# Kernel tuning notes

Hardware: AMD Instinct MI355X
Metric: run time of the kernel (lower is better)

The kernel has to match this reference:

```python
import jax, jax.numpy as jnp
import numpy as np

B, P, N = 2, 8192, 24
C1, C2 = 32, 32
K, A = 13, 12  # kernel points (12 anchors + center), rotation anchors


def _icosahedron_vs():
    phi = (1.0 + np.sqrt(5.0)) / 2.0
    v = []
    for s1 in (1.0, -1.0):
        for s2 in (1.0, -1.0):
            v.append([0.0, s1, s2 * phi])
            v.append([s1, s2 * phi, 0.0])
            v.append([s2 * phi, 0.0, s1])
    v = np.array(v, dtype=np.float32)
    return v / np.linalg.norm(v, axis=1, keepdims=True)


def setup_inputs() -> dict:
    key = jax.random.key(0)
    ks = jax.random.split(key, 6)
    rng = np.random.RandomState(0)
    vertices = jax.random.normal(ks[0], (B, P, 3), jnp.float32)
    neighbor_index = jax.random.randint(ks[1], (B, P, N), 0, P)
    feature_map = jax.random.normal(ks[2], (B, C1, K, P, A), jnp.float32)
    W = jax.random.normal(ks[3], (C2, C1, 36), jnp.float32) * 0.05
    bias = jax.random.normal(ks[4], (C2, 5), jnp.float32) * 0.05
    k_pos_w = jax.random.normal(ks[5], (C2, 36), jnp.float32) * 0.1
    vs = jnp.asarray(_icosahedron_vs())
    # precomputed rotation-group trace index buffers (valid-range stand-ins for
    # the fr.get_relativeV_index / idx_map precomputation in the original repo)
    idx_map = jnp.asarray(rng.randint(0, 36, size=(K * A,)), jnp.int32)          # [156] -> 36 classes
    trace_idxv_rot = jnp.asarray(np.stack([rng.permutation(K) for _ in range(A)]), jnp.int32)  # [A(r), K]
    trace_idx_rot = jnp.asarray(np.stack([rng.permutation(A) for _ in range(A)]), jnp.int32)   # [A(r), A]
    lvl = jnp.asarray(np.concatenate([rng.randint(0, 4, size=(A,)), np.array([4])]), jnp.int32)  # [K] shell level per kernel point
    return dict(neighbor_index=neighbor_index, vertices=vertices, feature_map=feature_map,
                W=W, bias=bias, k_pos_w=k_pos_w, vs=vs, idx_map=idx_map,
                trace_idxv_rot=trace_idxv_rot, trace_idx_rot=trace_idx_rot, lvl=lvl)


def reference(neighbor_index, vertices, feature_map, W, bias, k_pos_w, vs,
              idx_map, trace_idxv_rot, trace_idx_rot, lvl):
    c2, c1, _ = W.shape
    # unit-normalized neighbor directions: [b, p, n, 3]
    nbr = jax.vmap(lambda v, i: v[i])(vertices, neighbor_index)
    d = nbr - vertices[:, :, None, :]
    ndn = d / jnp.maximum(jnp.linalg.norm(d, axis=-1, keepdims=True), 1e-12)
    # expand the 36 equivariance classes to the full (k, a) kernel grid
    k_pos_w_ori = k_pos_w[:, idx_map].reshape(c2, K, A)        # [d, k, a]
    W_re = W[:, :, idx_map].reshape(c2, c1, K, A)              # [d, c, k, a]
    # rotate kernel-point and anchor axes per output rotation r (gather by trace idx)
    Ik = trace_idxv_rot[:, :, None]   # [r, k, 1], values in [0, K)
    Ia = trace_idx_rot[:, None, :]    # [r, 1, a], values in [0, A)
    W_eff = jnp.transpose(W_re[:, :, Ik, Ia], (0, 1, 3, 4, 2))   # [d, c, k, a, r]
    k_eff = jnp.transpose(k_pos_w_ori[:, Ik, Ia], (0, 2, 3, 1))  # [d, k, a, r]
    # learned kernel-point positions on S2 and positional weights vs local geometry
    k_pos_ori = jnp.einsum('dka,ac->dkc', k_pos_w_ori, vs)
    k_pos_ori = k_pos_ori / jnp.maximum(jnp.linalg.norm(k_pos_ori, axis=-1, keepdims=True), 1e-12)
    mean_dir = ndn.mean(axis=2)                                  # [b, p, 3]
    pw = jax.nn.relu(jnp.einsum('bpc,dkc->bdpk', mean_dir, k_pos_ori))
    # equivariant conv: small per-point matmul over (c, a) per kernel point, then k-weighted sum
    WT = W_eff * k_eff[:, None]                                  # [d, c, k, a, r]
    agg = jnp.einsum('dckar,bckpa->bdkpr', WT, feature_map)
    out = jnp.einsum('bdkpr,bdpk->bdpr', agg, pw)
    bias_eff = bias[:, lvl][:, trace_idxv_rot].sum(axis=-1)      # [d, r]
    return jax.nn.relu(out + bias_eff[None, :, None, :])
```

## Files before the change

kernel.cpp:

```cpp
#include <hip/hip_runtime.h>
#include <cstdint>
#include <cstddef>

#define B_   2
#define P_   8192
#define NN_  24
#define C1_  32
#define C2_  32
#define K_   13
#define A_   12
#define DR_  384
#define CA_  384
#define PT_  32
#define BPAD 408

typedef __attribute__((ext_vector_type(8))) short short8;
typedef __attribute__((ext_vector_type(4))) float floatx4;

__device__ __forceinline__ unsigned short f2bf(float f) {
    union { float f; unsigned int u; } v; v.f = f;
    unsigned int u = v.u;
    return (unsigned short)((u + 0x7fffu + ((u >> 16) & 1u)) >> 16);
}


__global__ void build_wt(const float* __restrict__ W, const float* __restrict__ kpw,
                         const int* __restrict__ idx_map, const int* __restrict__ tivr,
                         const int* __restrict__ tir, unsigned short* __restrict__ WT2) {
    int id = blockIdx.x * 256 + threadIdx.x;
    const int TOT = K_ * DR_ * CA_;
    if (id >= TOT) return;
    int ca = id % CA_;
    int t1 = id / CA_;
    int dr = t1 % DR_;
    int k  = t1 / DR_;
    int d = dr / 12, r = dr % 12;
    int c = ca / 12, a = ca % 12;
    int kk = tivr[r * K_ + k];
    int ia = tir[r * A_ + a];
    int m  = idx_map[kk * A_ + ia];
    WT2[id] = f2bf(W[(d * C1_ + c) * 36 + m] * kpw[d * 36 + m]);
}

__global__ void build_md(const int* __restrict__ nbr, const float* __restrict__ verts,
                         float* __restrict__ md) {
    int t = blockIdx.x * 256 + threadIdx.x;
    if (t >= B_ * P_) return;
    const float* vp = verts + (size_t)t * 3;
    float vx = vp[0], vy = vp[1], vz = vp[2];
    int b = t / P_;
    const int* np = nbr + (size_t)t * NN_;
    float ax = 0.f, ay = 0.f, az = 0.f;
    for (int n = 0; n < NN_; n++) {
        int j = np[n];
        const float* vq = verts + ((size_t)b * P_ + j) * 3;
        float dx = vq[0] - vx, dy = vq[1] - vy, dz = vq[2] - vz;
        float nn = sqrtf(dx * dx + dy * dy + dz * dz);
        float inv = 1.f / fmaxf(nn, 1e-12f);
        ax += dx * inv; ay += dy * inv; az += dz * inv;
    }
    const float s = 1.f / 24.f;
    md[t * 3 + 0] = ax * s; md[t * 3 + 1] = ay * s; md[t * 3 + 2] = az * s;
}

__global__ void build_kpo(const float* __restrict__ kpw, const int* __restrict__ idx_map,
                          const float* __restrict__ vs, float* __restrict__ kpo) {
    int t = blockIdx.x * 64 + threadIdx.x;
    if (t >= C2_ * K_) return;
    int d = t / K_, k = t % K_;
    float x = 0.f, y = 0.f, z = 0.f;
    for (int a = 0; a < A_; a++) {
        float w = kpw[d * 36 + idx_map[k * A_ + a]];
        x += w * vs[a * 3 + 0]; y += w * vs[a * 3 + 1]; z += w * vs[a * 3 + 2];
    }
    float nn = sqrtf(x * x + y * y + z * z);
    float inv = 1.f / fmaxf(nn, 1e-12f);
    kpo[t * 3 + 0] = x * inv; kpo[t * 3 + 1] = y * inv; kpo[t * 3 + 2] = z * inv;
}

__global__ void build_be(const float* __restrict__ bias, const int* __restrict__ lvl,
                         const int* __restrict__ tivr, float* __restrict__ be) {
    int t = blockIdx.x * 64 + threadIdx.x;
    if (t >= DR_) return;
    int d = t / 12, r = t % 12;
    float s = 0.f;
    for (int k = 0; k < K_; k++) s += bias[d * 5 + lvl[tivr[r * K_ + k]]];
    be[t] = s;
}

__global__ __launch_bounds__(256, 2) void main_gemm(
    const float* __restrict__ fm, const unsigned short* __restrict__ WT,
    const float* __restrict__ md, const float* __restrict__ kpo,
    const float* __restrict__ be, float* __restrict__ out) {

    __shared__ __attribute__((aligned(16))) unsigned short Bs[2][PT_][BPAD];
    __shared__ float pwS[2][PT_][C2_];
    __shared__ float mdS[PT_][3];
    __shared__ float kpoS[C2_ * K_ * 3];
    __shared__ float biasS[DR_];

    const int tid  = threadIdx.x;
    const int bid  = blockIdx.x;
    const int b    = bid >> 8;
    const int p0   = (bid & 255) << 5;
    const int lane = tid & 63;
    const int wid  = tid >> 6;
    const int rowm = lane & 15;
    const int quad = lane >> 4;

    float4 pf[12];
    int pf_c[12], pf_jj[12];
    #pragma unroll
    for (int j = 0; j < 12; j++) {
        int f = j * 256 + tid;
        pf_c[j]  = f / 96;
        pf_jj[j] = f - pf_c[j] * 96;
    }

    #define LOAD_PF(kk)                                                                  \
        { _Pragma("unroll")                                                              \
          for (int j = 0; j < 12; j++) {                                                 \
            const float4* src = (const float4*)(fm +                                     \
                ((((size_t)b * C1_ + pf_c[j]) * K_ + (kk)) * P_ + p0) * A_) + pf_jj[j];  \
            pf[j] = *src;                                                                \
          } }

    #define STORE_PF(bufw)                                                               \
        { _Pragma("unroll")                                                              \
          for (int j = 0; j < 12; j++) {                                                 \
            int pl = pf_jj[j] / 3, aseg = (pf_jj[j] - pl * 3) * 4;                       \
            ushort4 pk = make_ushort4(f2bf(pf[j].x), f2bf(pf[j].y),                      \
                                      f2bf(pf[j].z), f2bf(pf[j].w));                     \
            *(ushort4*)&Bs[bufw][pl][pf_c[j] * A_ + aseg] = pk;                          \
          } }

    #define CALC_PW(bufw, kk)                                                            \
        { for (int i = tid; i < C2_ * PT_; i += 256) {                                   \
            int d = i >> 5, pl = i & 31;                                                 \
            const float* kv = &kpoS[(d * K_ + (kk)) * 3];                                \
            float s = mdS[pl][0] * kv[0] + mdS[pl][1] * kv[1] + mdS[pl][2] * kv[2];      \
            pwS[bufw][pl][d] = fmaxf(s, 0.f);                                            \
          } }

    const unsigned short* awbase = WT + (size_t)(wid * 96 + rowm) * CA_ + quad * 8;
    #define LOAD_A(dst, kk, ch)                                                          \
        { const unsigned short* ap = awbase + (size_t)(kk) * (DR_ * CA_) + (ch) * 32;    \
          _Pragma("unroll")                                                              \
          for (int mt = 0; mt < 6; mt++) dst[mt] = *(const short8*)(ap + mt * 16 * CA_); }

    for (int i = tid; i < PT_ * 3; i += 256) {
        int p = i / 3, c = i % 3;
        mdS[p][c] = md[((size_t)b * P_ + p0 + p) * 3 + c];
    }
    for (int i = tid; i < C2_ * K_ * 3; i += 256) kpoS[i] = kpo[i];
    for (int i = tid; i < DR_; i += 256) biasS[i] = be[i];

    floatx4 acc_o[6][2];
    floatx4 acc_k[6][2];
    #pragma unroll
    for (int mt = 0; mt < 6; mt++)
        #pragma unroll
        for (int nt = 0; nt < 2; nt++) { acc_o[mt][nt] = (floatx4)0.f; acc_k[mt][nt] = (floatx4)0.f; }

    short8 abuf[2][6];

    LOAD_PF(0);
    __syncthreads();
    STORE_PF(0);
    CALC_PW(0, 0);
    LOAD_A(abuf[0], 0, 0);
    LOAD_PF(1);

    for (int k = 0; k < K_; k++) {
        const int buf = k & 1;
        __syncthreads();

        #pragma unroll
        for (int ch = 0; ch < 12; ch++) {
            if (ch < 11) LOAD_A(abuf[(ch + 1) & 1], k, ch + 1);
            short8 bfr[2];
            #pragma unroll
            for (int nt = 0; nt < 2; nt++)
                bfr[nt] = *(const short8*)(&Bs[buf][nt * 16 + rowm][ch * 32 + quad * 8]);
            const short8* af = abuf[ch & 1];
            #pragma unroll
            for (int mt = 0; mt < 6; mt++)
                #pragma unroll
                for (int nt = 0; nt < 2; nt++)
                    acc_k[mt][nt] = __builtin_amdgcn_mfma_f32_16x16x32_bf16(af[mt], bfr[nt], acc_k[mt][nt], 0, 0, 0);
        }

        #pragma unroll
        for (int mt = 0; mt < 6; mt++) {
            int drb = wid * 96 + mt * 16 + quad * 4;
            #pragma unroll
            for (int reg = 0; reg < 4; reg++) {
                int d = (drb + reg) / 12;
                #pragma unroll
                for (int nt = 0; nt < 2; nt++) {
                    float pv = pwS[buf][nt * 16 + rowm][d];
                    acc_o[mt][nt][reg] += pv * acc_k[mt][nt][reg];
                    acc_k[mt][nt][reg] = 0.f;
                }
            }
        }

        if (k + 1 < K_) {
            STORE_PF(buf ^ 1);
            CALC_PW(buf ^ 1, k + 1);
            LOAD_A(abuf[0], k + 1, 0);
        }
        if (k + 2 < K_) LOAD_PF(k + 2);
    }

    #pragma unroll
    for (int mt = 0; mt < 6; mt++) {
        #pragma unroll
        for (int reg = 0; reg < 4; reg++) {
            int dr = wid * 96 + mt * 16 + quad * 4 + reg;
            int d = dr / 12, r = dr - d * 12;
            #pragma unroll
            for (int nt = 0; nt < 2; nt++) {
                int p = p0 + nt * 16 + rowm;
                float v = acc_o[mt][nt][reg] + biasS[dr];
                out[(((size_t)b * C2_ + d) * P_ + p) * A_ + r] = fmaxf(v, 0.f);
            }
        }
    }
}

extern "C" void kernel_launch(void* const* d_in, const int* in_sizes, int n_in,
                              void* d_out, int out_size, void* d_ws, size_t ws_size,
                              hipStream_t stream) {
    const int*   nbr     = (const int*)d_in[0];
    const float* verts   = (const float*)d_in[1];
    const float* fm      = (const float*)d_in[2];
    const float* W       = (const float*)d_in[3];
    const float* bias    = (const float*)d_in[4];
    const float* kpw     = (const float*)d_in[5];
    const float* vs      = (const float*)d_in[6];
    const int*   idx_map = (const int*)d_in[7];
    const int*   tivr    = (const int*)d_in[8];
    const int*   tir     = (const int*)d_in[9];
    const int*   lvl     = (const int*)d_in[10];
    float* out = (float*)d_out;

    char* ws = (char*)d_ws;
    unsigned short* WT2 = (unsigned short*)ws;
    float* md_ws  = (float*)(ws + 4000000);
    float* kpo_ws = (float*)(ws + 4200000);
    float* be_ws  = (float*)(ws + 4210000);

    {
        const int TOT = K_ * DR_ * CA_;
        build_wt<<<(TOT + 255) / 256, 256, 0, stream>>>(W, kpw, idx_map, tivr, tir, WT2);
    }
    build_md<<<(B_ * P_) / 256, 256, 0, stream>>>(nbr, verts, md_ws);
    build_kpo<<<7, 64, 0, stream>>>(kpw, idx_map, vs, kpo_ws);
    build_be<<<6, 64, 0, stream>>>(bias, lvl, tivr, be_ws);

    main_gemm<<<B_ * (P_ / PT_), 256, 0, stream>>>(fm, WT2, md_ws, kpo_ws, be_ws, out);
}
```

Before: 734.5 us.

## Warp-specialize main GEMM with producer waves staging features, 64-point tiles

The main kernel now runs 512 threads: six consumer waves do only MFMA work, and two producer waves load the next kernel-point slice of the feature map, convert it to bf16 into shared memory and compute the positional weights. The point tile grows from 32 to 64, so each A-weight fragment is reused across four N tiles instead of two, and A loads are triple-buffered to prefetch two chunks ahead. The aim is to hide global feature loads behind compute and halve redundant weight traffic. The cost is a larger LDS footprint (~110KB per block), which may limit occupancy, and producer throughput may become the bottleneck with only two waves.

```diff
diff --git a/kernel.cpp b/kernel.cpp
--- a/kernel.cpp
+++ b/kernel.cpp
@@ -11,7 +11,7 @@
 #define A_   12
 #define DR_  384
 #define CA_  384
-#define PT_  32
+#define PT_  64
 #define BPAD 408
 
 typedef __attribute__((ext_vector_type(8))) short short8;
@@ -88,142 +88,144 @@
     be[t] = s;
 }
 
-__global__ __launch_bounds__(256, 2) void main_gemm(
+__global__ __launch_bounds__(512, 2) void main_gemm(
     const float* __restrict__ fm, const unsigned short* __restrict__ WT,
     const float* __restrict__ md, const float* __restrict__ kpo,
     const float* __restrict__ be, float* __restrict__ out) {
 
     __shared__ __attribute__((aligned(16))) unsigned short Bs[2][PT_][BPAD];
-    __shared__ float pwS[2][PT_][C2_];
+    __shared__ float pwS[2][PT_][33];
     __shared__ float mdS[PT_][3];
     __shared__ float kpoS[C2_ * K_ * 3];
     __shared__ float biasS[DR_];
 
     const int tid  = threadIdx.x;
     const int bid  = blockIdx.x;
-    const int b    = bid >> 8;
-    const int p0   = (bid & 255) << 5;
+    const int b    = bid >> 7;
+    const int p0   = (bid & 127) << 6;
     const int lane = tid & 63;
     const int wid  = tid >> 6;
     const int rowm = lane & 15;
     const int quad = lane >> 4;
-
-    float4 pf[12];
-    int pf_c[12], pf_jj[12];
-    #pragma unroll
-    for (int j = 0; j < 12; j++) {
-        int f = j * 256 + tid;
-        pf_c[j]  = f / 96;
-        pf_jj[j] = f - pf_c[j] * 96;
-    }
-
-    #define LOAD_PF(kk)                                                                  \
+    const bool consumer = (wid < 6);
+
+    #define PLOADR(dst, s, rr)                                                           \
         { _Pragma("unroll")                                                              \
-          for (int j = 0; j < 12; j++) {                                                 \
-            const float4* src = (const float4*)(fm +                                     \
-                ((((size_t)b * C1_ + pf_c[j]) * K_ + (kk)) * P_ + p0) * A_) + pf_jj[j];  \
-            pf[j] = *src;                                                                \
+          for (int jj = 0; jj < 12; jj++) {                                              \
+            int fi = (rr) * 1536 + jj * 128 + ptid;                                      \
+            int c = fi / 192; int j = fi - c * 192;                                      \
+            dst[jj] = *((const float4*)(fm +                                             \
+                ((((size_t)b * C1_ + c) * K_ + (s)) * P_ + p0) * A_) + j);               \
           } }
-
-    #define STORE_PF(bufw)                                                               \
+    #define PWRITE(src, bw, rr)                                                          \
         { _Pragma("unroll")                                                              \
-          for (int j = 0; j < 12; j++) {                                                 \
-            int pl = pf_jj[j] / 3, aseg = (pf_jj[j] - pl * 3) * 4;                       \
-            ushort4 pk = make_ushort4(f2bf(pf[j].x), f2bf(pf[j].y),                      \
-                                      f2bf(pf[j].z), f2bf(pf[j].w));                     \
-            *(ushort4*)&Bs[bufw][pl][pf_c[j] * A_ + aseg] = pk;                          \
+          for (int jj = 0; jj < 12; jj++) {                                              \
+            int fi = (rr) * 1536 + jj * 128 + ptid;                                      \
+            int c = fi / 192; int j = fi - c * 192;                                      \
+            int p = j / 3; int a4 = (j - p * 3) * 4;                                     \
+            ushort4 pk = make_ushort4(f2bf(src[jj].x), f2bf(src[jj].y),                  \
+                                      f2bf(src[jj].z), f2bf(src[jj].w));                 \
+            *(ushort4*)&Bs[bw][p][c * A_ + a4] = pk;                                     \
           } }
-
-    #define CALC_PW(bufw, kk)                                                            \
-        { for (int i = tid; i < C2_ * PT_; i += 256) {                                   \
-            int d = i >> 5, pl = i & 31;                                                 \
-            const float* kv = &kpoS[(d * K_ + (kk)) * 3];                                \
-            float s = mdS[pl][0] * kv[0] + mdS[pl][1] * kv[1] + mdS[pl][2] * kv[2];      \
-            pwS[bufw][pl][d] = fmaxf(s, 0.f);                                            \
+    #define PSTAGE(s, bw)                                                                \
+        { float4 pfA[12], pfB[12];                                                       \
+          PLOADR(pfA, s, 0); PLOADR(pfB, s, 1);                                          \
+          PWRITE(pfA, bw, 0);                                                            \
+          PLOADR(pfA, s, 2);                                                             \
+          PWRITE(pfB, bw, 1);                                                            \
+          PLOADR(pfB, s, 3);                                                             \
+          PWRITE(pfA, bw, 2);                                                            \
+          PWRITE(pfB, bw, 3);                                                            \
+          _Pragma("unroll")                                                              \
+          for (int t = 0; t < 16; t++) {                                                 \
+            int idx = t * 128 + ptid; int p = idx >> 5; int d = idx & 31;                \
+            const float* kv = &kpoS[(d * K_ + (s)) * 3];                                 \
+            float sd = mdS[p][0] * kv[0] + mdS[p][1] * kv[1] + mdS[p][2] * kv[2];        \
+            pwS[bw][p][d] = fmaxf(sd, 0.f);                                              \
           } }
 
-    const unsigned short* awbase = WT + (size_t)(wid * 96 + rowm) * CA_ + quad * 8;
+    const unsigned short* awbase = WT + (size_t)(wid * 64 + rowm) * CA_ + quad * 8;
     #define LOAD_A(dst, kk, ch)                                                          \
         { const unsigned short* ap = awbase + (size_t)(kk) * (DR_ * CA_) + (ch) * 32;    \
           _Pragma("unroll")                                                              \
-          for (int mt = 0; mt < 6; mt++) dst[mt] = *(const short8*)(ap + mt * 16 * CA_); }
-
-    for (int i = tid; i < PT_ * 3; i += 256) {
+          for (int mt = 0; mt < 4; mt++) dst[mt] = *(const short8*)(ap + mt * 16 * CA_); }
+
+    for (int i = tid; i < PT_ * 3; i += 512) {
         int p = i / 3, c = i % 3;
         mdS[p][c] = md[((size_t)b * P_ + p0 + p) * 3 + c];
     }
-    for (int i = tid; i < C2_ * K_ * 3; i += 256) kpoS[i] = kpo[i];
-    for (int i = tid; i < DR_; i += 256) biasS[i] = be[i];
-
-    floatx4 acc_o[6][2];
-    floatx4 acc_k[6][2];
-    #pragma unroll
-    for (int mt = 0; mt < 6; mt++)
+    for (int i = tid; i < C2_ * K_ * 3; i += 512) kpoS[i] = kpo[i];
+    for (int i = tid; i < DR_; i += 512) biasS[i] = be[i];
+    __syncthreads();
+
+    floatx4 acc_o[4][4];
+    floatx4 acc_k[4][4];
+    short8 abuf[3][4];
+    const int ptid = tid - 384;
+
+    if (consumer) {
         #pragma unroll
-        for (int nt = 0; nt < 2; nt++) { acc_o[mt][nt] = (floatx4)0.f; acc_k[mt][nt] = (floatx4)0.f; }
-
-    short8 abuf[2][6];
-
-    LOAD_PF(0);
+        for (int mt = 0; mt < 4; mt++)
+            #pragma unroll
+            for (int nt = 0; nt < 4; nt++) { acc_o[mt][nt] = (floatx4)0.f; acc_k[mt][nt] = (floatx4)0.f; }
+        LOAD_A(abuf[0], 0, 0);
+        LOAD_A(abuf[1], 0, 1);
+    } else {
+        PSTAGE(0, 0);
+    }
     __syncthreads();
-    STORE_PF(0);
-    CALC_PW(0, 0);
-    LOAD_A(abuf[0], 0, 0);
-    LOAD_PF(1);
 
     for (int k = 0; k < K_; k++) {
         const int buf = k & 1;
-        __syncthreads();
-
-        #pragma unroll
-        for (int ch = 0; ch < 12; ch++) {
-            if (ch < 11) LOAD_A(abuf[(ch + 1) & 1], k, ch + 1);
-            short8 bfr[2];
-            #pragma unroll
-            for (int nt = 0; nt < 2; nt++)
-                bfr[nt] = *(const short8*)(&Bs[buf][nt * 16 + rowm][ch * 32 + quad * 8]);
-            const short8* af = abuf[ch & 1];
-            #pragma unroll
-            for (int mt = 0; mt < 6; mt++)
-                #pragma unroll
-                for (int nt = 0; nt < 2; nt++)
-                    acc_k[mt][nt] = __builtin_amdgcn_mfma_f32_16x16x32_bf16(af[mt], bfr[nt], acc_k[mt][nt], 0, 0, 0);
-        }
-
-        #pragma unroll
-        for (int mt = 0; mt < 6; mt++) {
-            int drb = wid * 96 + mt * 16 + quad * 4;
-            #pragma unroll
-            for (int reg = 0; reg < 4; reg++) {
-                int d = (drb + reg) / 12;
-                #pragma unroll
-                for (int nt = 0; nt < 2; nt++) {
-                    float pv = pwS[buf][nt * 16 + rowm][d];
-                    acc_o[mt][nt][reg] += pv * acc_k[mt][nt][reg];
-                    acc_k[mt][nt][reg] = 0.f;
+        if (consumer) {
+            #pragma unroll
+            for (int ch = 0; ch < 12; ch++) {
+                if (ch < 10)          { LOAD_A(abuf[(ch + 2) % 3], k, ch + 2); }
+                else if (k + 1 < K_)  { LOAD_A(abuf[(ch + 2) % 3], k + 1, ch - 10); }
+                short8 bfr[4];
+                #pragma unroll
+                for (int nt = 0; nt < 4; nt++)
+                    bfr[nt] = *(const short8*)(&Bs[buf][nt * 16 + rowm][ch * 32 + quad * 8]);
+                const short8* af = abuf[ch % 3];
+                #pragma unroll
+                for (int mt = 0; mt < 4; mt++)
+                    #pragma unroll
+                    for (int nt = 0; nt < 4; nt++)
+                        acc_k[mt][nt] = __builtin_amdgcn_mfma_f32_16x16x32_bf16(af[mt], bfr[nt], acc_k[mt][nt], 0, 0, 0);
+            }
+            #pragma unroll
+            for (int mt = 0; mt < 4; mt++) {
+                int drb = wid * 64 + mt * 16 + quad * 4;
+                #pragma unroll
+                for (int reg = 0; reg < 4; reg++) {
+                    int d = (drb + reg) / 12;
+                    #pragma unroll
+                    for (int nt = 0; nt < 4; nt++) {
+                        float pv = pwS[buf][nt * 16 + rowm][d];
+                        acc_o[mt][nt][reg] += pv * acc_k[mt][nt][reg];
+                        acc_k[mt][nt][reg] = 0.f;
+                    }
                 }
             }
+        } else {
+            if (k + 1 < K_) { PSTAGE(k + 1, (k + 1) & 1); }
         }
-
-        if (k + 1 < K_) {
-            STORE_PF(buf ^ 1);
-            CALC_PW(buf ^ 1, k + 1);
-            LOAD_A(abuf[0], k + 1, 0);
-        }
-        if (k + 2 < K_) LOAD_PF(k + 2);
-    }
-
-    #pragma unroll
-    for (int mt = 0; mt < 6; mt++) {
+        __syncthreads();
+    }
+
+    if (consumer) {
         #pragma unroll
-        for (int reg = 0; reg < 4; reg++) {
-            int dr = wid * 96 + mt * 16 + quad * 4 + reg;
-            int d = dr / 12, r = dr - d * 12;
-            #pragma unroll
-            for (int nt = 0; nt < 2; nt++) {
-                int p = p0 + nt * 16 + rowm;
-                float v = acc_o[mt][nt][reg] + biasS[dr];
-                out[(((size_t)b * C2_ + d) * P_ + p) * A_ + r] = fmaxf(v, 0.f);
+        for (int mt = 0; mt < 4; mt++) {
+            #pragma unroll
+            for (int reg = 0; reg < 4; reg++) {
+                int dr = wid * 64 + mt * 16 + quad * 4 + reg;
+                int d = dr / 12, r = dr - d * 12;
+                #pragma unroll
+                for (int nt = 0; nt < 4; nt++) {
+                    int p = p0 + nt * 16 + rowm;
+                    float v = acc_o[mt][nt][reg] + biasS[dr];
+                    out[(((size_t)b * C2_ + d) * P_ + p) * A_ + r] = fmaxf(v, 0.f);
+                }
             }
         }
     }
@@ -259,5 +261,5 @@
     build_kpo<<<7, 64, 0, stream>>>(kpw, idx_map, vs, kpo_ws);
     build_be<<<6, 64, 0, stream>>>(bias, lvl, tivr, be_ws);
 
-    main_gemm<<<B_ * (P_ / PT_), 256, 0, stream>>>(fm, WT2, md_ws, kpo_ws, be_ws, out);
-}
+    main_gemm<<<B_ * (P_ / PT_), 512, 0, stream>>>(fm, WT2, md_ws, kpo_ws, be_ws, out);
+}
```

Measured after the change: 1.028 ms. 1.4x slower.
